# Optimization experiments

Measured on AMD Instinct MI355X. Metric: run time of the kernel, lower is better.

The kernel has to match this reference:

```python
import jax, jax.numpy as jnp
import numpy as np

M = 131072  # KV length
DK = 256    # key dim
DV = 256    # value dim


def setup_inputs() -> dict:
    key = jax.random.key(0)
    k1, k2, k3 = jax.random.split(key, 3)
    q = jax.random.normal(k1, (DK,), dtype=jnp.float32)
    K = jax.random.normal(k2, (M, DK), dtype=jnp.float32)
    V = jax.random.normal(k3, (M, DV), dtype=jnp.float32)
    return {"q": q, "K": K, "V": V}


def reference(q, K, V):
    # logits[m] = sum_k K[m,k] * q[k]
    logits = jnp.einsum('mk,k->m', K, q)
    # stable softmax over the m axis
    weights = jax.nn.softmax(logits, axis=-1)
    # y[v] = sum_m weights[m] * V[m,v]
    return jnp.einsum('m,mv->v', weights, V)
```

## Files before the change

### kernel.cpp

```cpp
#include <hip/hip_runtime.h>
#include <math.h>

#define DKD 256
#define DVD 256

constexpr int TPB = 256;
constexpr int NB  = 1024;
constexpr int RPB = 128;

__global__ __launch_bounds__(TPB, 4) void k_fused(
    const float* __restrict__ q,
    const float* __restrict__ K,
    const float* __restrict__ V,
    float* __restrict__ partT,
    float* __restrict__ pmax,
    float* __restrict__ psum)
{
    __shared__ __align__(16) float s_l[RPB];
    __shared__ float  s_wred[4];
    __shared__ float4 s_acc[4][64];

    const int t    = threadIdx.x;
    const int lane = t & 63;
    const int wave = t >> 6;
    const int b    = blockIdx.x;

    const float4* __restrict__ K4 = (const float4*)K;
    const float4* __restrict__ V4 = (const float4*)V;
    const float4 q4 = ((const float4*)q)[lane];

    const int wbeg = b * RPB + wave * (RPB / 4);

    float wmax = -INFINITY;
    #pragma unroll 2
    for (int it = 0; it < 8; ++it) {
        const int r = wbeg + it * 4;
        const size_t base = (size_t)r * 64 + lane;
        float4 k0 = K4[base];
        float4 k1 = K4[base + 64];
        float4 k2 = K4[base + 128];
        float4 k3 = K4[base + 192];

        float s0 = k0.x*q4.x + k0.y*q4.y + k0.z*q4.z + k0.w*q4.w;
        float s1 = k1.x*q4.x + k1.y*q4.y + k1.z*q4.z + k1.w*q4.w;
        float s2 = k2.x*q4.x + k2.y*q4.y + k2.z*q4.z + k2.w*q4.w;
        float s3 = k3.x*q4.x + k3.y*q4.y + k3.z*q4.z + k3.w*q4.w;

        #pragma unroll
        for (int off = 32; off > 0; off >>= 1) {
            s0 += __shfl_xor(s0, off);
            s1 += __shfl_xor(s1, off);
            s2 += __shfl_xor(s2, off);
            s3 += __shfl_xor(s3, off);
        }
        wmax = fmaxf(wmax, fmaxf(fmaxf(s0, s1), fmaxf(s2, s3)));
        if (lane < 4) {
            const float sv = lane == 0 ? s0 : lane == 1 ? s1 : lane == 2 ? s2 : s3;
            s_l[wave * 32 + it * 4 + lane] = sv;
        }
    }
    if (lane == 0) s_wred[wave] = wmax;
    __syncthreads();

    const float mb = fmaxf(fmaxf(s_wred[0], s_wred[1]), fmaxf(s_wred[2], s_wred[3]));

    if (t < RPB) s_l[t] = __expf(s_l[t] - mb);
    __syncthreads();
    if (wave == 0) {
        float es = s_l[lane] + s_l[lane + 64];
        #pragma unroll
        for (int off = 32; off > 0; off >>= 1) es += __shfl_xor(es, off);
        if (lane == 0) { pmax[b] = mb; psum[b] = es; }
    }

    float4 acc = make_float4(0.f, 0.f, 0.f, 0.f);
    const int ebase = wave * 32;
    #pragma unroll 2
    for (int it = 0; it < 8; ++it) {
        const int r = wbeg + it * 4;
        const size_t base = (size_t)r * 64 + lane;
        const float4 w4 = *(const float4*)&s_l[ebase + it * 4];
        float4 v0 = V4[base];
        float4 v1 = V4[base + 64];
        float4 v2 = V4[base + 128];
        float4 v3 = V4[base + 192];

        acc.x += w4.x*v0.x + w4.y*v1.x + w4.z*v2.x + w4.w*v3.x;
        acc.y += w4.x*v0.y + w4.y*v1.y + w4.z*v2.y + w4.w*v3.y;
        acc.z += w4.x*v0.z + w4.y*v1.z + w4.z*v2.z + w4.w*v3.z;
        acc.w += w4.x*v0.w + w4.y*v1.w + w4.z*v2.w + w4.w*v3.w;
    }

    s_acc[wave][lane] = acc;
    __syncthreads();
    float yv = 0.f;
    const float* saf = (const float*)&s_acc[0][0];
    #pragma unroll
    for (int ww = 0; ww < 4; ++ww) yv += saf[ww * DVD + t];
    partT[(size_t)t * NB + b] = yv;
}

__global__ __launch_bounds__(TPB) void k_combine(
    const float* __restrict__ partT,
    const float* __restrict__ pmax,
    const float* __restrict__ psum,
    float* __restrict__ out)
{
    __shared__ float red[TPB];
    __shared__ __align__(16) float s_a[NB];
    const int t = threadIdx.x;

    const float4 pm = ((const float4*)pmax)[t];
    float lm = fmaxf(fmaxf(pm.x, pm.y), fmaxf(pm.z, pm.w));
    red[t] = lm; __syncthreads();
    for (int s = TPB / 2; s > 0; s >>= 1) {
        if (t < s) red[t] = fmaxf(red[t], red[t + s]);
        __syncthreads();
    }
    const float Mg = red[0];
    __syncthreads();

    const float4 ps = ((const float4*)psum)[t];
    float4 a;
    a.x = __expf(pm.x - Mg); a.y = __expf(pm.y - Mg);
    a.z = __expf(pm.z - Mg); a.w = __expf(pm.w - Mg);
    ((float4*)s_a)[t] = a;
    red[t] = a.x*ps.x + a.y*ps.y + a.z*ps.z + a.w*ps.w;
    __syncthreads();
    for (int s = TPB / 2; s > 0; s >>= 1) {
        if (t < s) red[t] += red[t + s];
        __syncthreads();
    }
    const float invL = 1.0f / red[0];
    __syncthreads();

    const int j = blockIdx.x;
    const float4 v  = ((const float4*)(partT + (size_t)j * NB))[t];
    const float4 av = ((const float4*)s_a)[t];
    red[t] = v.x*av.x + v.y*av.y + v.z*av.z + v.w*av.w;
    __syncthreads();
    for (int s = TPB / 2; s > 0; s >>= 1) {
        if (t < s) red[t] += red[t + s];
        __syncthreads();
    }
    if (t == 0) out[j] = red[0] * invL;
}

extern "C" void kernel_launch(void* const* d_in, const int* in_sizes, int n_in,
                              void* d_out, int out_size, void* d_ws, size_t ws_size,
                              hipStream_t stream) {
    const float* q = (const float*)d_in[0];
    const float* K = (const float*)d_in[1];
    const float* V = (const float*)d_in[2];
    float* out = (float*)d_out;

    float* ws    = (float*)d_ws;
    float* partT = ws;
    float* pmax  = partT + (size_t)DVD * NB;
    float* psum  = pmax + NB;

    k_fused  <<<NB,  TPB, 0, stream>>>(q, K, V, partT, pmax, psum);
    k_combine<<<DVD, TPB, 0, stream>>>(partT, pmax, psum, out);
}
```

Baseline: 280.5 us.

## Replace per-row shuffle reductions with shared-memory transpose reduction and double block size

Each fused block now uses 512 threads (8 waves), so a wave handles 16 rows instead of 32. Instead of a 6-step butterfly shuffle for every row dot product, partial lane sums go into a skewed shared buffer. Four threads per row then reduce them with a few shuffles. This cuts cross-lane reduction work in the K phase at the cost of 32KB of LDS per block and an extra barrier, which may limit occupancy. The kernel is memory-bound on streaming K and V, so any gain depends on latency hiding.

```diff
diff --git a/kernel.cpp b/kernel.cpp
--- a/kernel.cpp
+++ b/kernel.cpp
@@ -4,11 +4,14 @@
 #define DKD 256
 #define DVD 256
 
-constexpr int TPB = 256;
-constexpr int NB  = 1024;
-constexpr int RPB = 128;
+constexpr int TPB  = 512;
+constexpr int NB   = 1024;
+constexpr int RPB  = 128;
+constexpr int WPB  = TPB / 64;
+constexpr int RPW  = RPB / WPB;
+constexpr int TPBC = 256;
 
-__global__ __launch_bounds__(TPB, 4) void k_fused(
+__global__ __launch_bounds__(TPB, 8) void k_fused(
     const float* __restrict__ q,
     const float* __restrict__ K,
     const float* __restrict__ V,
@@ -16,9 +19,9 @@
     float* __restrict__ pmax,
     float* __restrict__ psum)
 {
+    __shared__ __align__(16) float s_buf[RPB * 64];
     __shared__ __align__(16) float s_l[RPB];
-    __shared__ float  s_wred[4];
-    __shared__ float4 s_acc[4][64];
+    __shared__ float s_wred[WPB];
 
     const int t    = threadIdx.x;
     const int lane = t & 63;
@@ -29,13 +32,13 @@
     const float4* __restrict__ V4 = (const float4*)V;
     const float4 q4 = ((const float4*)q)[lane];
 
-    const int wbeg = b * RPB + wave * (RPB / 4);
+    const int lbeg = wave * RPW;
+    const int gbeg = b * RPB + lbeg;
 
-    float wmax = -INFINITY;
     #pragma unroll 2
-    for (int it = 0; it < 8; ++it) {
-        const int r = wbeg + it * 4;
-        const size_t base = (size_t)r * 64 + lane;
+    for (int it = 0; it < RPW / 4; ++it) {
+        const int lr = lbeg + it * 4;
+        const size_t base = (size_t)(gbeg + it * 4) * 64 + lane;
         float4 k0 = K4[base];
         float4 k1 = K4[base + 64];
         float4 k2 = K4[base + 128];
@@ -46,26 +49,37 @@
         float s2 = k2.x*q4.x + k2.y*q4.y + k2.z*q4.z + k2.w*q4.w;
         float s3 = k3.x*q4.x + k3.y*q4.y + k3.z*q4.z + k3.w*q4.w;
 
-        #pragma unroll
-        for (int off = 32; off > 0; off >>= 1) {
-            s0 += __shfl_xor(s0, off);
-            s1 += __shfl_xor(s1, off);
-            s2 += __shfl_xor(s2, off);
-            s3 += __shfl_xor(s3, off);
-        }
-        wmax = fmaxf(wmax, fmaxf(fmaxf(s0, s1), fmaxf(s2, s3)));
-        if (lane < 4) {
-            const float sv = lane == 0 ? s0 : lane == 1 ? s1 : lane == 2 ? s2 : s3;
-            s_l[wave * 32 + it * 4 + lane] = sv;
-        }
+        s_buf[(lr + 0) * 64 + ((lane + lr + 0) & 63)] = s0;
+        s_buf[(lr + 1) * 64 + ((lane + lr + 1) & 63)] = s1;
+        s_buf[(lr + 2) * 64 + ((lane + lr + 2) & 63)] = s2;
+        s_buf[(lr + 3) * 64 + ((lane + lr + 3) & 63)] = s3;
     }
-    if (lane == 0) s_wred[wave] = wmax;
     __syncthreads();
 
-    const float mb = fmaxf(fmaxf(s_wred[0], s_wred[1]), fmaxf(s_wred[2], s_wred[3]));
+    const int row = t >> 2;
+    const int qtr = t & 3;
+    float rs = 0.f;
+    const int cbase = qtr * 16;
+    #pragma unroll
+    for (int i = 0; i < 16; ++i)
+        rs += s_buf[row * 64 + ((cbase + i + row) & 63)];
+    rs += __shfl_xor(rs, 1);
+    rs += __shfl_xor(rs, 2);
+
+    float wm = rs;
+    #pragma unroll
+    for (int off = 4; off < 64; off <<= 1) wm = fmaxf(wm, __shfl_xor(wm, off));
+    if (lane == 0) s_wred[wave] = wm;
+    if (qtr == 0) s_l[row] = rs;
+    __syncthreads();
+
+    float mb = s_wred[0];
+    #pragma unroll
+    for (int wv = 1; wv < WPB; ++wv) mb = fmaxf(mb, s_wred[wv]);
 
     if (t < RPB) s_l[t] = __expf(s_l[t] - mb);
     __syncthreads();
+
     if (wave == 0) {
         float es = s_l[lane] + s_l[lane + 64];
         #pragma unroll
@@ -74,12 +88,10 @@
     }
 
     float4 acc = make_float4(0.f, 0.f, 0.f, 0.f);
-    const int ebase = wave * 32;
     #pragma unroll 2
-    for (int it = 0; it < 8; ++it) {
-        const int r = wbeg + it * 4;
-        const size_t base = (size_t)r * 64 + lane;
-        const float4 w4 = *(const float4*)&s_l[ebase + it * 4];
+    for (int it = 0; it < RPW / 4; ++it) {
+        const size_t base = (size_t)(gbeg + it * 4) * 64 + lane;
+        const float4 w4 = *(const float4*)&s_l[lbeg + it * 4];
         float4 v0 = V4[base];
         float4 v1 = V4[base + 64];
         float4 v2 = V4[base + 128];
@@ -91,29 +103,32 @@
         acc.w += w4.x*v0.w + w4.y*v1.w + w4.z*v2.w + w4.w*v3.w;
     }
 
-    s_acc[wave][lane] = acc;
+    float4* s_acc = (float4*)s_buf;
+    s_acc[wave * 64 + lane] = acc;
     __syncthreads();
-    float yv = 0.f;
-    const float* saf = (const float*)&s_acc[0][0];
-    #pragma unroll
-    for (int ww = 0; ww < 4; ++ww) yv += saf[ww * DVD + t];
-    partT[(size_t)t * NB + b] = yv;
+    if (t < DVD) {
+        const float* saf = (const float*)s_acc;
+        float yv = 0.f;
+        #pragma unroll
+        for (int wv = 0; wv < WPB; ++wv) yv += saf[wv * DVD + t];
+        partT[(size_t)t * NB + b] = yv;
+    }
 }
 
-__global__ __launch_bounds__(TPB) void k_combine(
+__global__ __launch_bounds__(TPBC) void k_combine(
     const float* __restrict__ partT,
     const float* __restrict__ pmax,
     const float* __restrict__ psum,
     float* __restrict__ out)
 {
-    __shared__ float red[TPB];
+    __shared__ float red[TPBC];
     __shared__ __align__(16) float s_a[NB];
     const int t = threadIdx.x;
 
     const float4 pm = ((const float4*)pmax)[t];
     float lm = fmaxf(fmaxf(pm.x, pm.y), fmaxf(pm.z, pm.w));
     red[t] = lm; __syncthreads();
-    for (int s = TPB / 2; s > 0; s >>= 1) {
+    for (int s = TPBC / 2; s > 0; s >>= 1) {
         if (t < s) red[t] = fmaxf(red[t], red[t + s]);
         __syncthreads();
     }
@@ -127,7 +142,7 @@
     ((float4*)s_a)[t] = a;
     red[t] = a.x*ps.x + a.y*ps.y + a.z*ps.z + a.w*ps.w;
     __syncthreads();
-    for (int s = TPB / 2; s > 0; s >>= 1) {
+    for (int s = TPBC / 2; s > 0; s >>= 1) {
         if (t < s) red[t] += red[t + s];
         __syncthreads();
     }
@@ -139,7 +154,7 @@
     const float4 av = ((const float4*)s_a)[t];
     red[t] = v.x*av.x + v.y*av.y + v.z*av.z + v.w*av.w;
     __syncthreads();
-    for (int s = TPB / 2; s > 0; s >>= 1) {
+    for (int s = TPBC / 2; s > 0; s >>= 1) {
         if (t < s) red[t] += red[t + s];
         __syncthreads();
     }
@@ -159,6 +174,6 @@
     float* pmax  = partT + (size_t)DVD * NB;
     float* psum  = pmax + NB;
 
-    k_fused  <<<NB,  TPB, 0, stream>>>(q, K, V, partT, pmax, psum);
-    k_combine<<<DVD, TPB, 0, stream>>>(partT, pmax, psum, out);
+    k_fused  <<<NB,   TPB,  0, stream>>>(q, K, V, partT, pmax, psum);
+    k_combine<<<DVD,  TPBC, 0, stream>>>(partT, pmax, psum, out);
 }
```

Result: no change. 279.7 us (-0.3%).
